# Kernel optimization log

Measured on AMD Instinct MI355X. Metric: run time of the kernel, lower is better.

The kernel has to match this reference:

```python
import jax, jax.numpy as jnp
from jax import lax
import numpy as np

B = 2
N_PER = 12000
TIMES = 16
C_IN = 4
# sparse_shape = grid_size[::-1] + [1,0,0], grid_size=[160,160,40]
S1 = (41, 160, 160)
S2 = (21, 80, 80)   # conv2: k3 s2 p1
S3 = (11, 40, 40)   # conv3: k3 s2 p1
S4 = (5, 20, 20)    # conv4: k3 s2 p(0,1,1)
SOUT = (2, 20, 20)  # conv_out: k(3,1,1) s(2,1,1) p0
# per-BN-layer channel counts, flattened into gamma/beta vectors
CH = [16, 16, 32, 32, 32, 64, 64, 64, 64, 64, 64, 128]
OFF = np.concatenate([[0], np.cumsum(CH)]).tolist()


def _downsample_coords(coords, in_shape, k, s, p):
    # spconv SparseConv3d output index rule: output j active iff some active
    # input x satisfies j*s - p <= x <= j*s - p + k - 1 within bounds.
    out_shape = np.array([(in_shape[i] + 2 * p[i] - k[i]) // s[i] + 1 for i in range(3)])
    b, xs = coords[:, :1], coords[:, 1:]
    s_arr = np.array(s)
    cand = []
    for o0 in range(k[0]):
        for o1 in range(k[1]):
            for o2 in range(k[2]):
                j = xs + np.array([p[0] - o0, p[1] - o1, p[2] - o2])
                ok = np.all(j % s_arr == 0, axis=1)
                jj = j // s_arr
                ok &= np.all((jj >= 0) & (jj < out_shape), axis=1)
                cand.append(np.concatenate([b[ok], jj[ok]], axis=1))
    return np.unique(np.concatenate(cand, axis=0), axis=0).astype(np.int32)


def _make_coords():
    rng = np.random.default_rng(0)
    ncell = S1[0] * S1[1] * S1[2]
    per = []
    for b in range(B):
        flat = rng.choice(ncell, size=N_PER, replace=False)
        z, y, x = np.unravel_index(flat, S1)
        per.append(np.stack([np.full(N_PER, b), z, y, x], axis=1))
    c1 = np.concatenate(per, axis=0).astype(np.int32)
    c2 = _downsample_coords(c1, S1, (3, 3, 3), (2, 2, 2), (1, 1, 1))
    c3 = _downsample_coords(c2, S2, (3, 3, 3), (2, 2, 2), (1, 1, 1))
    c4 = _downsample_coords(c3, S3, (3, 3, 3), (2, 2, 2), (0, 1, 1))
    c5 = _downsample_coords(c4, S4, (3, 1, 1), (2, 1, 1), (0, 0, 0))
    return c1, c2, c3, c4, c5


def _w(key, shape):
    fan_in = shape[0] * shape[1] * shape[2] * shape[3]
    return jax.random.normal(key, shape, jnp.float32) * np.float32(np.sqrt(2.0 / fan_in))


def setup_inputs():
    c1, c2, c3, c4, c5 = _make_coords()
    ks = jax.random.split(jax.random.key(0), 16)
    t = TIMES
    return {
        "voxel_features": jax.random.normal(ks[0], (c1.shape[0], C_IN), jnp.float32),
        "w_in": _w(ks[1], (3, 3, 3, C_IN, t)),
        "w1": _w(ks[2], (3, 3, 3, t, t)),
        "w2_0": _w(ks[3], (3, 3, 3, t, 2 * t)),
        "w2_1": _w(ks[4], (3, 3, 3, 2 * t, 2 * t)),
        "w2_2": _w(ks[5], (3, 3, 3, 2 * t, 2 * t)),
        "w3_0": _w(ks[6], (3, 3, 3, 2 * t, 4 * t)),
        "w3_1": _w(ks[7], (3, 3, 3, 4 * t, 4 * t)),
        "w3_2": _w(ks[8], (3, 3, 3, 4 * t, 4 * t)),
        "w4_0": _w(ks[9], (3, 3, 3, 4 * t, 4 * t)),
        "w4_1": _w(ks[10], (3, 3, 3, 4 * t, 4 * t)),
        "w4_2": _w(ks[11], (3, 3, 3, 4 * t, 4 * t)),
        "w_out": _w(ks[12], (3, 1, 1, 4 * t, 8 * t)),
        "gamma": 1.0 + 0.1 * jax.random.normal(ks[13], (sum(CH),), jnp.float32),
        "beta": 0.1 * jax.random.normal(ks[14], (sum(CH),), jnp.float32),
        "coords1": jnp.asarray(c1), "coords2": jnp.asarray(c2),
        "coords3": jnp.asarray(c3), "coords4": jnp.asarray(c4),
        "coords_out": jnp.asarray(c5),
    }


def _sp_conv(feats, in_coords, w, in_shape, out_coords, stride, padding):
    # spconv's rulebook gather->matmul->scatter over active sites computes the
    # same values as a dense conv on a zero-filled grid, read back only at the
    # active output coordinates (subm: out_coords == in_coords).
    dense = jnp.zeros((B,) + in_shape + (feats.shape[1],), feats.dtype)
    dense = dense.at[in_coords[:, 0], in_coords[:, 1], in_coords[:, 2], in_coords[:, 3]].set(feats)
    out = lax.conv_general_dilated(dense, w, window_strides=stride,
                                   padding=[(p, p) for p in padding],
                                   dimension_numbers=("NDHWC", "DHWIO", "NDHWC"))
    return out[out_coords[:, 0], out_coords[:, 1], out_coords[:, 2], out_coords[:, 3]]


def _bn_relu(x, g, b):
    # nn.BatchNorm1d(eps=1e-3) in training mode over the active voxels, + ReLU
    mu = jnp.mean(x, axis=0)
    var = jnp.mean(jnp.square(x - mu), axis=0)
    return jax.nn.relu((x - mu) * (g * lax.rsqrt(var + 1e-3)) + b)


def _forward(voxel_features, ws, gamma, beta, c1, c2, c3, c4, c5):
    layers = [
        (0, c1, S1, c1, (1, 1, 1), (1, 1, 1)),   # conv_input (subm, 4->16)
        (1, c1, S1, c1, (1, 1, 1), (1, 1, 1)),   # conv1 (subm)
        (2, c1, S1, c2, (2, 2, 2), (1, 1, 1)),   # conv2 spconv s2
        (3, c2, S2, c2, (1, 1, 1), (1, 1, 1)),
        (4, c2, S2, c2, (1, 1, 1), (1, 1, 1)),
        (5, c2, S2, c3, (2, 2, 2), (1, 1, 1)),   # conv3 spconv s2
        (6, c3, S3, c3, (1, 1, 1), (1, 1, 1)),
        (7, c3, S3, c3, (1, 1, 1), (1, 1, 1)),
        (8, c3, S3, c4, (2, 2, 2), (0, 1, 1)),   # conv4 spconv s2, pad (0,1,1)
        (9, c4, S4, c4, (1, 1, 1), (1, 1, 1)),
        (10, c4, S4, c4, (1, 1, 1), (1, 1, 1)),
        (11, c4, S4, c5, (2, 1, 1), (0, 0, 0)),  # conv_out k(3,1,1) s(2,1,1)
    ]
    x = voxel_features
    for i, ci, si, co, st, pd in layers:
        x = _sp_conv(x, ci, ws[i], si, co, st, pd)
        x = _bn_relu(x, gamma[OFF[i]:OFF[i + 1]], beta[OFF[i]:OFF[i + 1]])
    return x  # encoded_spconv_tensor features, [N_out, 8*times]


def reference(voxel_features, w_in, w1, w2_0, w2_1, w2_2, w3_0, w3_1, w3_2,
              w4_0, w4_1, w4_2, w_out, gamma, beta,
              coords1, coords2, coords3, coords4, coords_out):
    ws = [w_in, w1, w2_0, w2_1, w2_2, w3_0, w3_1, w3_2, w4_0, w4_1, w4_2, w_out]
    return _forward(voxel_features, ws, gamma, beta,
                    coords1, coords2, coords3, coords4, coords_out)
```

## Files before the change

### kernel.cpp

```cpp
#include <hip/hip_runtime.h>
#include <hip/hip_bf16.h>


typedef __attribute__((ext_vector_type(8))) short bf16x8;
typedef __attribute__((ext_vector_type(4))) short bf16x4s;
typedef __attribute__((ext_vector_type(4))) float f32x4;

typedef const __attribute__((address_space(1))) unsigned int* gas_ptr;
typedef __attribute__((address_space(3))) unsigned int* las_ptr;

__device__ __forceinline__ void dma16(const unsigned short* g, unsigned short* l) {
    __builtin_amdgcn_global_load_lds((gas_ptr)g, (las_ptr)l, 16, 0, 0);
}

__device__ inline unsigned short f2bf(float f) {
    unsigned u = __builtin_bit_cast(unsigned, f);
    u += 0x7FFFu + ((u >> 16) & 1u);
    return (unsigned short)(u >> 16);
}

struct ScatterArgs {
    const int* coords[4];
    int* grid[4];
    int n[4];
    int D[4], H[4], W[4];
};

__global__ __launch_bounds__(256) void scatter_grid_all(ScatterArgs a) {
    const int l = blockIdx.y;
    const int i = blockIdx.x * 256 + threadIdx.x;
    if (i >= a.n[l]) return;
    const int* c = a.coords[l] + 4 * i;
    a.grid[l][((c[0] * a.D[l] + c[1]) * a.H[l] + c[2]) * a.W[l] + c[3]] = i;
}

struct PrepArgs {
    const float* src[11];
    unsigned short* dst[11];
    int T[11], CIN[11], COUT[11], total[11];
};

__global__ __launch_bounds__(256) void prep_w_all(PrepArgs a) {
    const int l = blockIdx.y;
    const int i = blockIdx.x * 256 + threadIdx.x;
    if (i >= a.total[l]) return;
    const int COUT = a.COUT[l], CIN = a.CIN[l], T = a.T[l];
    const int co = i % COUT; const int r = i / COUT; const int ci = r % CIN; const int t = r / CIN;
    unsigned short v = (t < T) ? f2bf(a.src[l][i]) : (unsigned short)0;
    a.dst[l][((size_t)t * COUT + co) * CIN + ci] = v;
}

__global__ __launch_bounds__(256, 4) void sp_conv0(const float* __restrict__ fin,
                                                   const int* __restrict__ grid,
                                                   const int* __restrict__ oc, int n_out,
                                                   const float* __restrict__ w,
                                                   float* __restrict__ out,
                                                   int D, int H, int W) {
    const int c = threadIdx.x & 15;
    const int p = (blockIdx.x * 256 + threadIdx.x) >> 4;
    if (p >= n_out) return;
    const int b   = oc[4*p+0];
    const int iz0 = oc[4*p+1] - 1;
    const int iy0 = oc[4*p+2] - 1;
    const int ix0 = oc[4*p+3] - 1;
    const int* gb = grid + b * (D * H * W);
    float acc = 0.f;
    for (int kd = 0; kd < 3; ++kd) {
        const int iz = iz0 + kd;
        if ((unsigned)iz >= (unsigned)D) continue;
        for (int kh = 0; kh < 3; ++kh) {
            const int iy = iy0 + kh;
            if ((unsigned)iy >= (unsigned)H) continue;
            for (int kw = 0; kw < 3; ++kw) {
                const int ix = ix0 + kw;
                if ((unsigned)ix >= (unsigned)W) continue;
                const int idx = gb[(iz*H + iy)*W + ix];
                if (idx < 0) continue;
                const float4 v = *(const float4*)(fin + (size_t)idx * 4);
                const float* wp = w + (size_t)((kd*3 + kh)*3 + kw) * 64 + c;
                acc = fmaf(v.x, wp[0],  acc);
                acc = fmaf(v.y, wp[16], acc);
                acc = fmaf(v.z, wp[32], acc);
                acc = fmaf(v.w, wp[48], acc);
            }
        }
    }
    out[(size_t)p*16 + c] = acc;
}

template<int COUT>
__global__ __launch_bounds__(256, 4) void sp_conv16(
    const unsigned short* __restrict__ fin, const int* __restrict__ grid,
    const int* __restrict__ oc, int n_out,
    const unsigned short* __restrict__ wt, float* __restrict__ out,
    float* __restrict__ stats,
    int D, int H, int W, int sz, int sy, int sx, int pz, int py, int px)
{
    constexpr int T = 27;
    constexpr int KB = 14;
    __shared__ float ls[32];
    const int lane  = threadIdx.x & 63;
    const int wid   = threadIdx.x >> 6;
    const int n     = lane & 15;
    const int quad  = lane >> 4;
    const int cbase = blockIdx.y * 16;
    const int pbase = blockIdx.x * 64 + wid * 16;

    if (threadIdx.x < 32) ls[threadIdx.x] = 0.f;

    int pc = pbase + n;
    if (pc > n_out - 1) pc = n_out - 1;
    const int4 cc = ((const int4*)oc)[pc];
    const int* gb = grid + cc.x * (D * H * W);
    const int iz0 = cc.y * sz - pz;
    const int iy0 = cc.z * sy - py;
    const int ix0 = cc.w * sx - px;

    f32x4 acc = (f32x4){0.f, 0.f, 0.f, 0.f};
    const int cinb = (quad & 1) * 8;
    int idx[KB];
#pragma unroll
    for (int kb = 0; kb < KB; ++kb) {
        const int tap = 2*kb + (quad >> 1);
        const int te = tap < T ? tap : 0;
        const int kd = te/9, kr = te%9, kh = kr/3, kw = kr%3;
        const int iz = iz0 + kd, iy = iy0 + kh, ix = ix0 + kw;
        const bool ok = (tap < T) && (unsigned)iz < (unsigned)D &&
                        (unsigned)iy < (unsigned)H && (unsigned)ix < (unsigned)W;
        const int cz = iz < 0 ? 0 : (iz >= D ? D-1 : iz);
        const int cy = iy < 0 ? 0 : (iy >= H ? H-1 : iy);
        const int cx = ix < 0 ? 0 : (ix >= W ? W-1 : ix);
        const int g = gb[(cz*H + cy)*W + cx];
        idx[kb] = ok ? g : -1;
    }
#pragma unroll
    for (int k0 = 0; k0 < KB; k0 += 7) {
        bf16x8 a[7], b[7];
#pragma unroll
        for (int j = 0; j < 7; ++j)
            a[j] = *(const bf16x8*)(fin + (ptrdiff_t)idx[k0+j]*16 + cinb);
#pragma unroll
        for (int j = 0; j < 7; ++j) {
            const int tap = 2*(k0+j) + (quad >> 1);
            const int tw = tap < T ? tap : T;
            b[j] = *(const bf16x8*)(wt + ((size_t)tw*COUT + cbase + n)*16 + cinb);
        }
        __builtin_amdgcn_sched_barrier(0);
#pragma unroll
        for (int j = 0; j < 7; ++j)
            acc = __builtin_amdgcn_mfma_f32_16x16x32_bf16(a[j], b[j], acc, 0, 0, 0);
    }

#pragma unroll
    for (int r = 0; r < 4; ++r) {
        const int p = pbase + quad*4 + r;
        if (p < n_out) out[(size_t)p * COUT + cbase + n] = acc[r];
    }
    __syncthreads();
    {
        float s1 = 0.f, s2 = 0.f;
#pragma unroll
        for (int r = 0; r < 4; ++r) {
            const int p = pbase + quad*4 + r;
            if (p < n_out) { const float v = acc[r]; s1 += v; s2 += v*v; }
        }
        s1 += __shfl_xor(s1, 16); s2 += __shfl_xor(s2, 16);
        s1 += __shfl_xor(s1, 32); s2 += __shfl_xor(s2, 32);
        if (quad == 0) { atomicAdd(&ls[n], s1); atomicAdd(&ls[16+n], s2); }
    }
    __syncthreads();
    if (threadIdx.x < 16)
        atomicAdd(&stats[cbase + threadIdx.x], ls[threadIdx.x]);
    else if (threadIdx.x < 32)
        atomicAdd(&stats[COUT + cbase + (threadIdx.x - 16)], ls[threadIdx.x]);
}

template<int CIN, int COUT, int BT, int KD, int KH, int KW>
__global__ __launch_bounds__(256, 2) void sp_conv_lds(
    const unsigned short* __restrict__ fin, const int* __restrict__ grid,
    const int* __restrict__ oc, int n_out,
    const unsigned short* __restrict__ wt, float* __restrict__ out,
    float* __restrict__ stats,
    int D, int H, int W, int sz, int sy, int sx, int pz, int py, int px)
{
    constexpr int T    = KD*KH*KW;
    constexpr int TP   = ((T + BT - 1)/BT)*BT;
    constexpr int NT   = COUT/16;
    constexpr int S    = CIN/32;
    constexpr int LPR  = CIN/8;
    constexpr int RPD  = 64/LPR;
    constexpr int ADMA = 16/RPD;
    constexpr int BDMA = COUT/RPD;

    __shared__ unsigned short Abuf[4*BT*16*CIN];
    __shared__ unsigned short Bbuf[BT*COUT*CIN];
    __shared__ float ls[2*COUT];

    const int l     = threadIdx.x & 63;
    const int w     = threadIdx.x >> 6;
    const int n     = l & 15;
    const int quad  = l >> 4;
    const int pbase = blockIdx.x * 64 + w * 16;

    if (threadIdx.x < 2*COUT) ls[threadIdx.x] = 0.f;

    int pc = pbase + n;
    if (pc > n_out - 1) pc = n_out - 1;
    const int4 cc = ((const int4*)oc)[pc];
    const int* gb = grid + cc.x * (D * H * W);
    const int iz0 = cc.y * sz - pz;
    const int iy0 = cc.z * sy - py;
    const int ix0 = cc.w * sx - px;

    int idx[TP];
#pragma unroll
    for (int tap = 0; tap < TP; ++tap) {
        const int te = tap < T ? tap : 0;
        const int kd = te/(KH*KW), kr = te%(KH*KW), kh = kr/KW, kw = kr%KW;
        const int iz = iz0 + kd, iy = iy0 + kh, ix = ix0 + kw;
        const bool ok = (tap < T) && (unsigned)iz < (unsigned)D &&
                        (unsigned)iy < (unsigned)H && (unsigned)ix < (unsigned)W;
        const int cz = iz < 0 ? 0 : (iz >= D ? D-1 : iz);
        const int cy = iy < 0 ? 0 : (iy >= H ? H-1 : iy);
        const int cx = ix < 0 ? 0 : (ix >= W ? W-1 : ix);
        const int g = gb[(cz*H + cy)*W + cx];
        idx[tap] = ok ? g : -1;
    }

    f32x4 acc[NT];
#pragma unroll
    for (int t = 0; t < NT; ++t) acc[t] = (f32x4){0.f, 0.f, 0.f, 0.f};

#pragma unroll
    for (int tb0 = 0; tb0 < TP; tb0 += BT) {
#pragma unroll
        for (int j = 0; j < BT; ++j) {
#pragma unroll
            for (int d = 0; d < ADMA; ++d) {
                const int m  = d*RPD + l/LPR;
                const int i0 = __shfl(idx[tb0+j], m, 16);
                const int slot = (l % LPR) ^ (m % LPR);
                const unsigned short* gp = fin + (ptrdiff_t)i0*CIN + slot*8;
                unsigned short* lp = Abuf + ((w*BT + j)*16 + d*RPD)*CIN;
                dma16(gp, lp);
            }
        }
        for (int q = w; q < BT*BDMA; q += 4) {
            const int j = q / BDMA, d = q % BDMA;
            const int t = tb0 + j;
            const int tw = t < T ? t : T;
            const int r  = d*RPD + l/LPR;
            const int slot = (l % LPR) ^ (r % LPR);
            const unsigned short* gp = wt + ((size_t)tw*COUT + r)*CIN + slot*8;
            unsigned short* lp = Bbuf + (j*COUT + d*RPD)*CIN;
            dma16(gp, lp);
        }
        __syncthreads();
#pragma unroll
        for (int j = 0; j < BT; ++j) {
            const unsigned short* Aw = Abuf + (w*BT + j)*16*CIN;
            const unsigned short* Bw = Bbuf + j*COUT*CIN;
#pragma unroll
            for (int s = 0; s < S; ++s) {
                const int c = s*4 + quad;
                bf16x8 a = *(const bf16x8*)(Aw + n*CIN + ((c ^ (n % LPR)) * 8));
#pragma unroll
                for (int t = 0; t < NT; ++t) {
                    const int r = t*16 + n;
                    bf16x8 b = *(const bf16x8*)(Bw + r*CIN + ((c ^ (r % LPR)) * 8));
                    acc[t] = __builtin_amdgcn_mfma_f32_16x16x32_bf16(a, b, acc[t], 0, 0, 0);
                }
            }
        }
        __syncthreads();
    }

#pragma unroll
    for (int t = 0; t < NT; ++t)
#pragma unroll
        for (int r = 0; r < 4; ++r) {
            const int p = pbase + quad*4 + r;
            if (p < n_out) out[(size_t)p * COUT + t*16 + n] = acc[t][r];
        }

#pragma unroll
    for (int t = 0; t < NT; ++t) {
        float s1 = 0.f, s2 = 0.f;
#pragma unroll
        for (int r = 0; r < 4; ++r) {
            const int p = pbase + quad*4 + r;
            if (p < n_out) { const float v = acc[t][r]; s1 += v; s2 += v*v; }
        }
        s1 += __shfl_xor(s1, 16); s2 += __shfl_xor(s2, 16);
        s1 += __shfl_xor(s1, 32); s2 += __shfl_xor(s2, 32);
        if (quad == 0) {
            atomicAdd(&ls[t*16 + n], s1);
            atomicAdd(&ls[COUT + t*16 + n], s2);
        }
    }
    __syncthreads();
    if (threadIdx.x < 2*COUT) atomicAdd(&stats[threadIdx.x], ls[threadIdx.x]);
}

template<int C>
__global__ __launch_bounds__(256) void reduce_stats(const float* __restrict__ x, int nn,
                                                    float* __restrict__ stats)
{
    constexpr int R = 256 / C;
    __shared__ float s1[256];
    __shared__ float s2[256];
    const int c = threadIdx.x % C;
    const int r = threadIdx.x / C;
    float a1 = 0.f, a2 = 0.f;
    for (int i = blockIdx.x * R + r; i < nn; i += R * gridDim.x) {
        float v = x[(size_t)i*C + c];
        a1 += v;
        a2 += v * v;
    }
    s1[threadIdx.x] = a1;
    s2[threadIdx.x] = a2;
    __syncthreads();
    for (int off = 128; off >= C; off >>= 1) {
        if (threadIdx.x < off) {
            s1[threadIdx.x] += s1[threadIdx.x + off];
            s2[threadIdx.x] += s2[threadIdx.x + off];
        }
        __syncthreads();
    }
    if (threadIdx.x < C) {
        atomicAdd(&stats[c],     s1[threadIdx.x]);
        atomicAdd(&stats[C + c], s2[threadIdx.x]);
    }
}

__device__ inline void stv4(float* p, float4 v) { *(float4*)p = v; }
__device__ inline void stv4(unsigned short* p, float4 v) {
    bf16x4s o;
    o.x = (short)f2bf(v.x); o.y = (short)f2bf(v.y);
    o.z = (short)f2bf(v.z); o.w = (short)f2bf(v.w);
    *(bf16x4s*)p = o;
}

template<int C, typename OUT>
__global__ __launch_bounds__(256) void bn_relu_apply(const float* __restrict__ x,
                                                     OUT* __restrict__ y, int nn,
                                                     const float* __restrict__ stats,
                                                     const float* __restrict__ gamma,
                                                     const float* __restrict__ beta)
{
    const size_t q = (size_t)blockIdx.x * blockDim.x + threadIdx.x;
    if (q >= (size_t)nn * (C/4)) return;
    const int c = (int)(q % (size_t)(C/4)) * 4;
    const float inv_n = 1.f / (float)nn;
    const float4 xv = *(const float4*)(x + q*4);
    const float4 s1 = *(const float4*)(stats + c);
    const float4 s2 = *(const float4*)(stats + C + c);
    const float4 gm = *(const float4*)(gamma + c);
    const float4 bt = *(const float4*)(beta + c);
    float4 o;
    { float mu=s1.x*inv_n, var=s2.x*inv_n-mu*mu, g=gm.x*rsqrtf(var+1e-3f);
      float v=(xv.x-mu)*g+bt.x; o.x = v>0.f? v:0.f; }
    { float mu=s1.y*inv_n, var=s2.y*inv_n-mu*mu, g=gm.y*rsqrtf(var+1e-3f);
      float v=(xv.y-mu)*g+bt.y; o.y = v>0.f? v:0.f; }
    { float mu=s1.z*inv_n, var=s2.z*inv_n-mu*mu, g=gm.z*rsqrtf(var+1e-3f);
      float v=(xv.z-mu)*g+bt.z; o.z = v>0.f? v:0.f; }
    { float mu=s1.w*inv_n, var=s2.w*inv_n-mu*mu, g=gm.w*rsqrtf(var+1e-3f);
      float v=(xv.w-mu)*g+bt.w; o.w = v>0.f? v:0.f; }
    stv4(y + q*4, o);
}

extern "C" void kernel_launch(void* const* d_in, const int* in_sizes, int n_in,
                              void* d_out, int out_size, void* d_ws, size_t ws_size,
                              hipStream_t stream) {
    const float* WPTR[12] = {
        (const float*)d_in[1], (const float*)d_in[2], (const float*)d_in[3],
        (const float*)d_in[4], (const float*)d_in[5], (const float*)d_in[6],
        (const float*)d_in[7], (const float*)d_in[8], (const float*)d_in[9],
        (const float*)d_in[10], (const float*)d_in[11], (const float*)d_in[12] };
    const float* vf    = (const float*)d_in[0];
    const float* gamma = (const float*)d_in[13];
    const float* beta  = (const float*)d_in[14];
    const int* c1 = (const int*)d_in[15];
    const int* c2 = (const int*)d_in[16];
    const int* c3 = (const int*)d_in[17];
    const int* c4 = (const int*)d_in[18];
    const int* c5 = (const int*)d_in[19];
    const int N1 = in_sizes[15] / 4;
    const int N2 = in_sizes[16] / 4;
    const int N3 = in_sizes[17] / 4;
    const int N4 = in_sizes[18] / 4;
    const int N5 = in_sizes[19] / 4;

    static const int LT[12]  = {27,27,27,27,27,27,27,27,27,27,27,3};
    static const int LCI[12] = {4,16,16,32,32,32,64,64,64,64,64,64};
    static const int LCO[12] = {16,16,32,32,32,64,64,64,64,64,64,128};

    const size_t G1 = (size_t)2*41*160*160;
    const size_t G2 = (size_t)2*21*80*80;
    const size_t G3 = (size_t)2*11*40*40;
    const size_t G4 = (size_t)2*5*20*20;
    int* grid1 = (int*)d_ws;
    int* grid2 = grid1 + G1;
    int* grid3 = grid2 + G2;
    int* grid4 = grid3 + G3;
    float* stats = (float*)(grid4 + G4);

    size_t maxE = (size_t)N1*16;
    if ((size_t)N2*32  > maxE) maxE = (size_t)N2*32;
    if ((size_t)N3*64  > maxE) maxE = (size_t)N3*64;
    if ((size_t)N4*64  > maxE) maxE = (size_t)N4*64;
    if ((size_t)N5*128 > maxE) maxE = (size_t)N5*128;
    maxE = (maxE + 7) & ~(size_t)7;

    float* raw = stats + 12*256;
    unsigned short* padA = (unsigned short*)(raw + maxE);
    unsigned short* fA   = padA + 128;
    unsigned short* padB = fA + maxE;
    unsigned short* fB   = padB + 128;
    unsigned short* wtb  = fB + maxE;
    size_t wtoff[12];
    {
        size_t o = 0;
        for (int i = 1; i < 12; ++i) {
            wtoff[i] = o;
            o += (size_t)(LT[i] + 1) * LCI[i] * LCO[i];
        }
    }

    hipMemsetAsync(grid1, 0xFF, (G1+G2+G3+G4)*sizeof(int), stream);
    hipMemsetAsync(stats, 0, 12*256*sizeof(float), stream);
    hipMemsetAsync(padA, 0, 128*sizeof(unsigned short), stream);
    hipMemsetAsync(padB, 0, 128*sizeof(unsigned short), stream);

    {
        ScatterArgs sa;
        sa.coords[0]=c1; sa.coords[1]=c2; sa.coords[2]=c3; sa.coords[3]=c4;
        sa.grid[0]=grid1; sa.grid[1]=grid2; sa.grid[2]=grid3; sa.grid[3]=grid4;
        sa.n[0]=N1; sa.n[1]=N2; sa.n[2]=N3; sa.n[3]=N4;
        sa.D[0]=41; sa.H[0]=160; sa.W[0]=160;
        sa.D[1]=21; sa.H[1]= 80; sa.W[1]= 80;
        sa.D[2]=11; sa.H[2]= 40; sa.W[2]= 40;
        sa.D[3]= 5; sa.H[3]= 20; sa.W[3]= 20;
        int mx = N1; if (N2>mx) mx=N2; if (N3>mx) mx=N3; if (N4>mx) mx=N4;
        dim3 g((mx + 255)/256, 4);
        scatter_grid_all<<<g, 256, 0, stream>>>(sa);
    }
    {
        PrepArgs pa;
        int mx = 0;
        for (int i = 1; i < 12; ++i) {
            pa.src[i-1] = WPTR[i];
            pa.dst[i-1] = wtb + wtoff[i];
            pa.T[i-1] = LT[i]; pa.CIN[i-1] = LCI[i]; pa.COUT[i-1] = LCO[i];
            pa.total[i-1] = (LT[i]+1)*LCI[i]*LCO[i];
            if (pa.total[i-1] > mx) mx = pa.total[i-1];
        }
        dim3 g((mx + 255)/256, 11);
        prep_w_all<<<g, 256, 0, stream>>>(pa);
    }

    enum { GOFF_0 = 0, GOFF_1 = 16, GOFF_2 = 32, GOFF_3 = 64, GOFF_4 = 96, GOFF_5 = 128,
           GOFF_6 = 192, GOFF_7 = 256, GOFF_8 = 320, GOFF_9 = 384, GOFF_10 = 448, GOFF_11 = 512 };

#define APPLY(i, COUT, NP, FOUT_T, FOUT) \
    bn_relu_apply<COUT, FOUT_T><<<(((size_t)(NP)*(COUT)/4) + 255)/256, 256, 0, stream>>>( \
        raw, FOUT, NP, stats + (i)*256, gamma + GOFF_##i, beta + GOFF_##i);

    sp_conv0<<<((size_t)N1*16 + 255)/256, 256, 0, stream>>>(vf, grid1, c1, N1, WPTR[0], raw, 41,160,160);
    { int rb = (N1 + 15)/16; if (rb > 240) rb = 240;
      reduce_stats<16><<<rb, 256, 0, stream>>>(raw, N1, stats + 0*256); }
    APPLY(0, 16, N1, unsigned short, fA);

#define CONV16(i, COUT, FIN, GRD, OC, NP, D,H,W, SZ,SY,SX, PZ,PY,PX) \
    { dim3 g_(((NP)+63)/64, (COUT)/16); \
      sp_conv16<COUT><<<g_, 256, 0, stream>>>( \
          FIN, GRD, OC, NP, wtb + wtoff[i], raw, stats + (i)*256, D,H,W, SZ,SY,SX, PZ,PY,PX); }

#define CONVL(i, CIN, COUT, BT, KD,KH,KW, FIN, GRD, OC, NP, D,H,W, SZ,SY,SX, PZ,PY,PX) \
    sp_conv_lds<CIN,COUT,BT,KD,KH,KW><<<((NP)+63)/64, 256, 0, stream>>>( \
        FIN, GRD, OC, NP, wtb + wtoff[i], raw, stats + (i)*256, D,H,W, SZ,SY,SX, PZ,PY,PX);

    CONV16( 1, 16,       fA, grid1, c1, N1, 41,160,160, 1,1,1, 1,1,1); APPLY( 1, 16, N1, unsigned short, fB);
    CONV16( 2, 32,       fB, grid1, c2, N2, 41,160,160, 2,2,2, 1,1,1); APPLY( 2, 32, N2, unsigned short, fA);
    CONVL ( 3, 32, 32, 7, 3,3,3, fA, grid2, c2, N2, 21, 80, 80, 1,1,1, 1,1,1); APPLY( 3, 32, N2, unsigned short, fB);
    CONVL ( 4, 32, 32, 7, 3,3,3, fB, grid2, c2, N2, 21, 80, 80, 1,1,1, 1,1,1); APPLY( 4, 32, N2, unsigned short, fA);
    CONVL ( 5, 32, 64, 7, 3,3,3, fA, grid2, c3, N3, 21, 80, 80, 2,2,2, 1,1,1); APPLY( 5, 64, N3, unsigned short, fB);
    CONVL ( 6, 64, 64, 3, 3,3,3, fB, grid3, c3, N3, 11, 40, 40, 1,1,1, 1,1,1); APPLY( 6, 64, N3, unsigned short, fA);
    CONVL ( 7, 64, 64, 3, 3,3,3, fA, grid3, c3, N3, 11, 40, 40, 1,1,1, 1,1,1); APPLY( 7, 64, N3, unsigned short, fB);
    CONVL ( 8, 64, 64, 3, 3,3,3, fB, grid3, c4, N4, 11, 40, 40, 2,2,2, 0,1,1); APPLY( 8, 64, N4, unsigned short, fA);
    CONVL ( 9, 64, 64, 3, 3,3,3, fA, grid4, c4, N4,  5, 20, 20, 1,1,1, 1,1,1); APPLY( 9, 64, N4, unsigned short, fB);
    CONVL (10, 64, 64, 3, 3,3,3, fB, grid4, c4, N4,  5, 20, 20, 1,1,1, 1,1,1); APPLY(10, 64, N4, unsigned short, fA);
    CONVL (11, 64,128, 1, 3,1,1, fA, grid4, c5, N5,  5, 20, 20, 2,1,1, 0,0,0); APPLY(11, 128, N5, float, (float*)d_out);
#undef CONV16
#undef CONVL
#undef APPLY
}
```

Before: 419.6 us.

## Stage CIN=16 conv gathers through LDS with async DMA and compute all output tiles per block

Replaces the direct-register-gather CIN=16 sparse conv with an LDS-staged version that uses global_load_lds DMA for gathered rows and weights, and computes every 16-wide output tile in one block instead of splitting output channels across grid.y. This avoids redundant neighbor-index lookups and input gathers per output-channel tile. It also restricts the grid index lookup to one quad per wave in both conv kernels, using full-wave shuffles to broadcast indices. The cost is extra syncthreads per tap batch and LDS traffic.

```diff
diff --git a/kernel.cpp b/kernel.cpp
--- a/kernel.cpp
+++ b/kernel.cpp
@@ -89,90 +89,129 @@
 }
 
 template<int COUT>
-__global__ __launch_bounds__(256, 4) void sp_conv16(
+__global__ __launch_bounds__(256, 4) void sp_conv_lds16(
     const unsigned short* __restrict__ fin, const int* __restrict__ grid,
     const int* __restrict__ oc, int n_out,
     const unsigned short* __restrict__ wt, float* __restrict__ out,
     float* __restrict__ stats,
     int D, int H, int W, int sz, int sy, int sx, int pz, int py, int px)
 {
-    constexpr int T = 27;
-    constexpr int KB = 14;
-    __shared__ float ls[32];
-    const int lane  = threadIdx.x & 63;
-    const int wid   = threadIdx.x >> 6;
-    const int n     = lane & 15;
-    const int quad  = lane >> 4;
-    const int cbase = blockIdx.y * 16;
-    const int pbase = blockIdx.x * 64 + wid * 16;
-
-    if (threadIdx.x < 32) ls[threadIdx.x] = 0.f;
-
-    int pc = pbase + n;
-    if (pc > n_out - 1) pc = n_out - 1;
-    const int4 cc = ((const int4*)oc)[pc];
-    const int* gb = grid + cc.x * (D * H * W);
-    const int iz0 = cc.y * sz - pz;
-    const int iy0 = cc.z * sy - py;
-    const int ix0 = cc.w * sx - px;
-
-    f32x4 acc = (f32x4){0.f, 0.f, 0.f, 0.f};
-    const int cinb = (quad & 1) * 8;
-    int idx[KB];
-#pragma unroll
-    for (int kb = 0; kb < KB; ++kb) {
-        const int tap = 2*kb + (quad >> 1);
-        const int te = tap < T ? tap : 0;
-        const int kd = te/9, kr = te%9, kh = kr/3, kw = kr%3;
-        const int iz = iz0 + kd, iy = iy0 + kh, ix = ix0 + kw;
-        const bool ok = (tap < T) && (unsigned)iz < (unsigned)D &&
-                        (unsigned)iy < (unsigned)H && (unsigned)ix < (unsigned)W;
-        const int cz = iz < 0 ? 0 : (iz >= D ? D-1 : iz);
-        const int cy = iy < 0 ? 0 : (iy >= H ? H-1 : iy);
-        const int cx = ix < 0 ? 0 : (ix >= W ? W-1 : ix);
-        const int g = gb[(cz*H + cy)*W + cx];
-        idx[kb] = ok ? g : -1;
-    }
-#pragma unroll
-    for (int k0 = 0; k0 < KB; k0 += 7) {
-        bf16x8 a[7], b[7];
-#pragma unroll
-        for (int j = 0; j < 7; ++j)
-            a[j] = *(const bf16x8*)(fin + (ptrdiff_t)idx[k0+j]*16 + cinb);
-#pragma unroll
-        for (int j = 0; j < 7; ++j) {
-            const int tap = 2*(k0+j) + (quad >> 1);
-            const int tw = tap < T ? tap : T;
-            b[j] = *(const bf16x8*)(wt + ((size_t)tw*COUT + cbase + n)*16 + cinb);
-        }
-        __builtin_amdgcn_sched_barrier(0);
-#pragma unroll
-        for (int j = 0; j < 7; ++j)
-            acc = __builtin_amdgcn_mfma_f32_16x16x32_bf16(a[j], b[j], acc, 0, 0, 0);
-    }
-
-#pragma unroll
-    for (int r = 0; r < 4; ++r) {
-        const int p = pbase + quad*4 + r;
-        if (p < n_out) out[(size_t)p * COUT + cbase + n] = acc[r];
-    }
-    __syncthreads();
-    {
-        float s1 = 0.f, s2 = 0.f;
+    constexpr int T  = 27;
+    constexpr int BT = 4;
+    constexpr int TP = 28;
+    constexpr int NT = COUT/16;
+    constexpr int NB = (COUT == 16) ? BT/2 : BT;
+
+    __shared__ unsigned short Abuf[4*BT*16*16];
+    __shared__ unsigned short Bbuf[BT*COUT*16];
+    __shared__ float ls[2*COUT];
+
+    const int l     = threadIdx.x & 63;
+    const int w     = threadIdx.x >> 6;
+    const int n     = l & 15;
+    const int quad  = l >> 4;
+    const int pbase = blockIdx.x * 64 + w * 16;
+
+    if (threadIdx.x < 2*COUT) ls[threadIdx.x] = 0.f;
+
+    int idx[TP];
+    if (quad == 0) {
+        int pc = pbase + n;
+        if (pc > n_out - 1) pc = n_out - 1;
+        const int4 cc = ((const int4*)oc)[pc];
+        const int* gb = grid + cc.x * (D * H * W);
+        const int iz0 = cc.y * sz - pz;
+        const int iy0 = cc.z * sy - py;
+        const int ix0 = cc.w * sx - px;
+#pragma unroll
+        for (int tap = 0; tap < TP; ++tap) {
+            const int te = tap < T ? tap : 0;
+            const int kd = te/9, kr = te%9, kh = kr/3, kw = kr%3;
+            const int iz = iz0 + kd, iy = iy0 + kh, ix = ix0 + kw;
+            const bool ok = (tap < T) && (unsigned)iz < (unsigned)D &&
+                            (unsigned)iy < (unsigned)H && (unsigned)ix < (unsigned)W;
+            const int cz = iz < 0 ? 0 : (iz >= D ? D-1 : iz);
+            const int cy = iy < 0 ? 0 : (iy >= H ? H-1 : iy);
+            const int cx = ix < 0 ? 0 : (ix >= W ? W-1 : ix);
+            const int g = gb[(cz*H + cy)*W + cx];
+            idx[tap] = ok ? g : -1;
+        }
+    }
+
+    f32x4 acc[NT];
+#pragma unroll
+    for (int t = 0; t < NT; ++t) acc[t] = (f32x4){0.f, 0.f, 0.f, 0.f};
+
+    const int h  = l >> 5;
+    const int m  = (l >> 1) & 15;
+    const int ch = l & 1;
+
+#pragma unroll
+    for (int tb0 = 0; tb0 < TP; tb0 += BT) {
+#pragma unroll
+        for (int q = 0; q < BT/2; ++q) {
+            const int v0 = __shfl(idx[tb0 + 2*q],     m);
+            const int v1 = __shfl(idx[tb0 + 2*q + 1], m);
+            const int row = h ? v1 : v0;
+            const unsigned short* gp = fin + (ptrdiff_t)row*16 + ch*8;
+            unsigned short* lp = Abuf + (w*BT + 2*q)*16*16;
+            dma16(gp, lp);
+        }
+        for (int q = w; q < NB; q += 4) {
+            if constexpr (COUT == 16) {
+                const int tap = tb0 + 2*q + h;
+                const int tw = tap < T ? tap : T;
+                const unsigned short* gp = wt + ((size_t)tw*COUT + m)*16 + ch*8;
+                unsigned short* lp = Bbuf + (2*q)*COUT*16;
+                dma16(gp, lp);
+            } else {
+                const int tap = tb0 + q;
+                const int tw = tap < T ? tap : T;
+                const int r = l >> 1;
+                const unsigned short* gp = wt + ((size_t)tw*COUT + r)*16 + ch*8;
+                unsigned short* lp = Bbuf + q*COUT*16;
+                dma16(gp, lp);
+            }
+        }
+        __syncthreads();
+#pragma unroll
+        for (int jp = 0; jp < BT/2; ++jp) {
+            const int ts = 2*jp + (quad >> 1);
+            bf16x8 a = *(const bf16x8*)(Abuf + ((w*BT + ts)*16 + n)*16 + (quad & 1)*8);
+#pragma unroll
+            for (int t = 0; t < NT; ++t) {
+                bf16x8 b = *(const bf16x8*)(Bbuf + (ts*COUT + t*16 + n)*16 + (quad & 1)*8);
+                acc[t] = __builtin_amdgcn_mfma_f32_16x16x32_bf16(a, b, acc[t], 0, 0, 0);
+            }
+        }
+        __syncthreads();
+    }
+
+#pragma unroll
+    for (int t = 0; t < NT; ++t)
 #pragma unroll
         for (int r = 0; r < 4; ++r) {
             const int p = pbase + quad*4 + r;
-            if (p < n_out) { const float v = acc[r]; s1 += v; s2 += v*v; }
+            if (p < n_out) out[(size_t)p * COUT + t*16 + n] = acc[t][r];
+        }
+
+#pragma unroll
+    for (int t = 0; t < NT; ++t) {
+        float s1 = 0.f, s2 = 0.f;
+#pragma unroll
+        for (int r = 0; r < 4; ++r) {
+            const int p = pbase + quad*4 + r;
+            if (p < n_out) { const float v = acc[t][r]; s1 += v; s2 += v*v; }
         }
         s1 += __shfl_xor(s1, 16); s2 += __shfl_xor(s2, 16);
         s1 += __shfl_xor(s1, 32); s2 += __shfl_xor(s2, 32);
-        if (quad == 0) { atomicAdd(&ls[n], s1); atomicAdd(&ls[16+n], s2); }
+        if (quad == 0) {
+            atomicAdd(&ls[t*16 + n], s1);
+            atomicAdd(&ls[COUT + t*16 + n], s2);
+        }
     }
     __syncthreads();
-    if (threadIdx.x < 16)
-        atomicAdd(&stats[cbase + threadIdx.x], ls[threadIdx.x]);
-    else if (threadIdx.x < 32)
-        atomicAdd(&stats[COUT + cbase + (threadIdx.x - 16)], ls[threadIdx.x]);
+    if (threadIdx.x < 2*COUT) atomicAdd(&stats[threadIdx.x], ls[threadIdx.x]);
 }
 
 template<int CIN, int COUT, int BT, int KD, int KH, int KW>
@@ -204,27 +243,28 @@
 
     if (threadIdx.x < 2*COUT) ls[threadIdx.x] = 0.f;
 
-    int pc = pbase + n;
-    if (pc > n_out - 1) pc = n_out - 1;
-    const int4 cc = ((const int4*)oc)[pc];
-    const int* gb = grid + cc.x * (D * H * W);
-    const int iz0 = cc.y * sz - pz;
-    const int iy0 = cc.z * sy - py;
-    const int ix0 = cc.w * sx - px;
-
     int idx[TP];
-#pragma unroll
-    for (int tap = 0; tap < TP; ++tap) {
-        const int te = tap < T ? tap : 0;
-        const int kd = te/(KH*KW), kr = te%(KH*KW), kh = kr/KW, kw = kr%KW;
-        const int iz = iz0 + kd, iy = iy0 + kh, ix = ix0 + kw;
-        const bool ok = (tap < T) && (unsigned)iz < (unsigned)D &&
-                        (unsigned)iy < (unsigned)H && (unsigned)ix < (unsigned)W;
-        const int cz = iz < 0 ? 0 : (iz >= D ? D-1 : iz);
-        const int cy = iy < 0 ? 0 : (iy >= H ? H-1 : iy);
-        const int cx = ix < 0 ? 0 : (ix >= W ? W-1 : ix);
-        const int g = gb[(cz*H + cy)*W + cx];
-        idx[tap] = ok ? g : -1;
+    if (quad == 0) {
+        int pc = pbase + n;
+        if (pc > n_out - 1) pc = n_out - 1;
+        const int4 cc = ((const int4*)oc)[pc];
+        const int* gb = grid + cc.x * (D * H * W);
+        const int iz0 = cc.y * sz - pz;
+        const int iy0 = cc.z * sy - py;
+        const int ix0 = cc.w * sx - px;
+#pragma unroll
+        for (int tap = 0; tap < TP; ++tap) {
+            const int te = tap < T ? tap : 0;
+            const int kd = te/(KH*KW), kr = te%(KH*KW), kh = kr/KW, kw = kr%KW;
+            const int iz = iz0 + kd, iy = iy0 + kh, ix = ix0 + kw;
+            const bool ok = (tap < T) && (unsigned)iz < (unsigned)D &&
+                            (unsigned)iy < (unsigned)H && (unsigned)ix < (unsigned)W;
+            const int cz = iz < 0 ? 0 : (iz >= D ? D-1 : iz);
+            const int cy = iy < 0 ? 0 : (iy >= H ? H-1 : iy);
+            const int cx = ix < 0 ? 0 : (ix >= W ? W-1 : ix);
+            const int g = gb[(cz*H + cy)*W + cx];
+            idx[tap] = ok ? g : -1;
+        }
     }
 
     f32x4 acc[NT];
@@ -238,7 +278,7 @@
 #pragma unroll
             for (int d = 0; d < ADMA; ++d) {
                 const int m  = d*RPD + l/LPR;
-                const int i0 = __shfl(idx[tb0+j], m, 16);
+                const int i0 = __shfl(idx[tb0+j], m);
                 const int slot = (l % LPR) ^ (m % LPR);
                 const unsigned short* gp = fin + (ptrdiff_t)i0*CIN + slot*8;
                 unsigned short* lp = Abuf + ((w*BT + j)*16 + d*RPD)*CIN;
@@ -471,17 +511,16 @@
       reduce_stats<16><<<rb, 256, 0, stream>>>(raw, N1, stats + 0*256); }
     APPLY(0, 16, N1, unsigned short, fA);
 
-#define CONV16(i, COUT, FIN, GRD, OC, NP, D,H,W, SZ,SY,SX, PZ,PY,PX) \
-    { dim3 g_(((NP)+63)/64, (COUT)/16); \
-      sp_conv16<COUT><<<g_, 256, 0, stream>>>( \
-          FIN, GRD, OC, NP, wtb + wtoff[i], raw, stats + (i)*256, D,H,W, SZ,SY,SX, PZ,PY,PX); }
+#define CONVS(i, COUT, FIN, GRD, OC, NP, D,H,W, SZ,SY,SX, PZ,PY,PX) \
+    sp_conv_lds16<COUT><<<((NP)+63)/64, 256, 0, stream>>>( \
+        FIN, GRD, OC, NP, wtb + wtoff[i], raw, stats + (i)*256, D,H,W, SZ,SY,SX, PZ,PY,PX);
 
 #define CONVL(i, CIN, COUT, BT, KD,KH,KW, FIN, GRD, OC, NP, D,H,W, SZ,SY,SX, PZ,PY,PX) \
     sp_conv_lds<CIN,COUT,BT,KD,KH,KW><<<((NP)+63)/64, 256, 0, stream>>>( \
         FIN, GRD, OC, NP, wtb + wtoff[i], raw, stats + (i)*256, D,H,W, SZ,SY,SX, PZ,PY,PX);
 
-    CONV16( 1, 16,       fA, grid1, c1, N1, 41,160,160, 1,1,1, 1,1,1); APPLY( 1, 16, N1, unsigned short, fB);
-    CONV16( 2, 32,       fB, grid1, c2, N2, 41,160,160, 2,2,2, 1,1,1); APPLY( 2, 32, N2, unsigned short, fA);
+    CONVS( 1, 16,       fA, grid1, c1, N1, 41,160,160, 1,1,1, 1,1,1); APPLY( 1, 16, N1, unsigned short, fB);
+    CONVS( 2, 32,       fB, grid1, c2, N2, 41,160,160, 2,2,2, 1,1,1); APPLY( 2, 32, N2, unsigned short, fA);
     CONVL ( 3, 32, 32, 7, 3,3,3, fA, grid2, c2, N2, 21, 80, 80, 1,1,1, 1,1,1); APPLY( 3, 32, N2, unsigned short, fB);
     CONVL ( 4, 32, 32, 7, 3,3,3, fB, grid2, c2, N2, 21, 80, 80, 1,1,1, 1,1,1); APPLY( 4, 32, N2, unsigned short, fA);
     CONVL ( 5, 32, 64, 7, 3,3,3, fA, grid2, c3, N3, 21, 80, 80, 2,2,2, 1,1,1); APPLY( 5, 64, N3, unsigned short, fB);
@@ -491,7 +530,7 @@
     CONVL ( 9, 64, 64, 3, 3,3,3, fA, grid4, c4, N4,  5, 20, 20, 1,1,1, 1,1,1); APPLY( 9, 64, N4, unsigned short, fB);
     CONVL (10, 64, 64, 3, 3,3,3, fB, grid4, c4, N4,  5, 20, 20, 1,1,1, 1,1,1); APPLY(10, 64, N4, unsigned short, fA);
     CONVL (11, 64,128, 1, 3,1,1, fA, grid4, c5, N5,  5, 20, 20, 2,1,1, 0,0,0); APPLY(11, 128, N5, float, (float*)d_out);
-#undef CONV16
+#undef CONVS
 #undef CONVL
 #undef APPLY
 }
```

Result: faster. 407.4 us (-2.9%).
